# Kernel optimization log

Hardware: AMD Instinct MI355X
Metric: run time of the kernel (lower is better)

Reference implementation:

```python
import jax, jax.numpy as jnp
import numpy as np

B, T_H, N, F_P = 16, 24, 256, 6
H, PRED_LEN, F_W = 64, 12, 4


def _build_static(coords):
    # haversine distance matrix -> gaussian kernel -> threshold (epsilon=0.5)
    lon, lat = coords[:, 0], coords[:, 1]
    dlon = lon[None, :] - lon[:, None]
    dlat = lat[None, :] - lat[:, None]
    a = (np.sin(np.radians(dlat / 2)) ** 2
         + np.cos(np.radians(lat[:, None])) * np.cos(np.radians(lat[None, :]))
         * np.sin(np.radians(dlon / 2)) ** 2)
    dist = 2.0 * 6371.0 * np.arcsin(np.sqrt(np.clip(a, 0.0, None)))
    std = dist.flatten().std()
    adj = np.exp(-np.square(dist / std))
    adj[adj < 0.5] = 0.0
    return adj.astype(np.float32)


def setup_inputs() -> dict:
    key = jax.random.key(0)
    ks = jax.random.split(key, 16)
    rng = np.random.default_rng(0)
    coords_np = np.stack([116.0 + rng.uniform(-1.0, 1.0, N),
                          40.0 + rng.uniform(-1.0, 1.0, N)], axis=1).astype(np.float32)
    s = 0.05
    scale_w = jnp.asarray([1.0, 360.0, 10.0, 1.0], jnp.float32)  # [_, dir(deg), speed, _]
    return {
        "history_pollution": jax.random.normal(ks[0], (B, T_H, N, F_P), jnp.float32),
        "history_weather": jax.random.uniform(ks[1], (B, T_H, F_W), jnp.float32) * scale_w,
        "static_adj": jnp.asarray(_build_static(coords_np)),
        "coords": jnp.asarray(coords_np),
        "w_gc1": jax.random.normal(ks[2], (H, F_P), jnp.float32) * s,
        "b_gc1": jax.random.normal(ks[3], (H,), jnp.float32) * s,
        "w_gc2": jax.random.normal(ks[4], (H, H), jnp.float32) * s,
        "b_gc2": jax.random.normal(ks[5], (H,), jnp.float32) * s,
        "w_ih": jax.random.normal(ks[6], (3 * H, H), jnp.float32) * s,
        "w_hh": jax.random.normal(ks[7], (3 * H, H), jnp.float32) * s,
        "b_ih": jax.random.normal(ks[8], (3 * H,), jnp.float32) * s,
        "b_hh": jax.random.normal(ks[9], (3 * H,), jnp.float32) * s,
        "w_m1": jax.random.normal(ks[10], (32, H), jnp.float32) * s,
        "b_m1": jax.random.normal(ks[11], (32,), jnp.float32) * s,
        "w_m2": jax.random.normal(ks[12], (F_P, 32), jnp.float32) * s,
        "b_m2": jax.random.normal(ks[13], (F_P,), jnp.float32) * s,
    }


def _forward(history_pollution, history_weather, static_adj, coords,
             w_gc1, b_gc1, w_gc2, b_gc2, w_ih, w_hh, b_ih, b_hh,
             w_m1, b_m1, w_m2, b_m2):
    Bs, Th, Ns, Fp = history_pollution.shape
    dt = history_pollution.dtype
    eye = jnp.eye(Ns, dtype=dt)
    # station pair angles: vecs[i,j] = coords[j] - coords[i]
    vecs = coords[None, :, :] - coords[:, None, :]
    ang = jnp.arctan2(vecs[..., 1], vecs[..., 0])  # [N,N]

    def gconv(x, adj, w, b):
        wt = adj + eye[None]                         # [B,N,N]
        d = 1.0 / (jnp.sqrt(wt.sum(-1)) + 1e-6)      # [B,N]
        norm = d[:, :, None] * wt * d[:, None, :]    # D^-1/2 W D^-1/2
        return jnp.einsum('bij,bjf->bif', norm, x) @ w.T + b

    def gcb(x, w_out, w_in):
        h1 = jax.nn.relu(gconv(x, w_out, w_gc1, b_gc1))
        return jax.nn.relu(gconv(h1, w_in, w_gc2, b_gc2))

    def gru(h, x):                                   # h,x: [B*N,H]
        gi = x @ w_ih.T + b_ih
        gh = h @ w_hh.T + b_hh
        i_r, i_z, i_n = jnp.split(gi, 3, axis=-1)
        h_r, h_z, h_n = jnp.split(gh, 3, axis=-1)
        r = jax.nn.sigmoid(i_r + h_r)
        z = jax.nn.sigmoid(i_z + h_z)
        n = jnp.tanh(i_n + r * h_n)
        return (1.0 - z) * n + z * h

    def mlp(x):
        return jax.nn.relu(x @ w_m1.T + b_m1) @ w_m2.T + b_m2

    def enc_step(carry, xs):
        h, _ = carry
        x_t, spd, wd = xs                            # [B,N,F],[B],[B]
        rad = jnp.deg2rad(wd)
        w_dyn = jnp.maximum(spd[:, None, None] * jnp.cos(ang[None] - rad[:, None, None]), 0.0)
        w_out = static_adj[None] * w_dyn             # [B,N,N]
        sf = gcb(x_t, w_out, jnp.swapaxes(w_out, 1, 2))
        h = gru(h, sf.reshape(Bs * Ns, -1))
        return (h, w_out), None

    h0 = jnp.zeros((Bs * Ns, w_hh.shape[1]), dt)
    xs = (jnp.moveaxis(history_pollution, 1, 0),      # [T,B,N,F]
          history_weather[:, :, 2].T,                 # wind speed [T,B]
          history_weather[:, :, 1].T)                 # wind dir   [T,B]
    (h, last_w_out), _ = jax.lax.scan(enc_step, (h0, jnp.zeros((Bs, Ns, Ns), dt)), xs)
    last_w_in = jnp.swapaxes(last_w_out, 1, 2)

    dec0 = mlp(h.reshape(Bs, Ns, -1))

    def dec_step(carry, _):
        h_c, x = carry
        sf = gcb(x, last_w_out, last_w_in)
        h_c = gru(h_c, sf.reshape(Bs * Ns, -1))
        pred = mlp(h_c.reshape(Bs, Ns, -1))
        return (h_c, pred), pred

    _, preds = jax.lax.scan(dec_step, (h, dec0), None, length=PRED_LEN)
    return jnp.moveaxis(preds, 0, 1)                  # [B, pred_len, N, F_P]


def reference(history_pollution, history_weather, static_adj, coords,
              w_gc1, b_gc1, w_gc2, b_gc2, w_ih, w_hh, b_ih, b_hh,
              w_m1, b_m1, w_m2, b_m2):
    return _forward(history_pollution, history_weather, static_adj, coords,
                    w_gc1, b_gc1, w_gc2, b_gc2, w_ih, w_hh, b_ih, b_hh,
                    w_m1, b_m1, w_m2, b_m2)
```

## Files before the change

kernel.cpp:

```cpp
#include <hip/hip_runtime.h>
#include <math.h>

#define Bsz 16
#define Tt 24
#define Nn 256
#define Fp 6
#define Hh 64
#define PredL 12
#define Fw 4
#define M1 32
#define TCHUNK 8
#define DEG2RAD 0.017453292519943295f
#define IDX2(t, b) ((t) * Bsz + (b))

__global__ __launch_bounds__(256) void k_prep(
    const float* __restrict__ coords, const float* __restrict__ adj,
    const float* __restrict__ wgc2, const float* __restrict__ wih,
    const float* __restrict__ whh,  const float* __restrict__ wm1,
    const float* __restrict__ wm2,
    float2* __restrict__ pk,
    float* __restrict__ wgc2T, float* __restrict__ wm1T, float* __restrict__ wm2T,
    float4* __restrict__ wihP, float4* __restrict__ whhP) {
  int tid = threadIdx.x;
  if (blockIdx.x < Nn) {
    int i = blockIdx.x;
    int j = tid;
    float dx = coords[2 * j]     - coords[2 * i];
    float dy = coords[2 * j + 1] - coords[2 * i + 1];
    float ang = atan2f(dy, dx);
    float a = adj[i * Nn + j];
    pk[i * Nn + j] = make_float2(a * cosf(ang), a * sinf(ang));
    return;
  }
  for (int idx = tid; idx < Hh * Hh; idx += 256) {
    int g = idx / Hh, k = idx % Hh;
    wgc2T[k * Hh + g] = wgc2[g * Hh + k];
  }
  for (int idx = tid; idx < M1 * Hh; idx += 256) {
    int m = idx / Hh, k = idx % Hh;
    wm1T[k * M1 + m] = wm1[m * Hh + k];
  }
  for (int idx = tid; idx < Fp * M1; idx += 256) {
    int f = idx / M1, m = idx % M1;
    wm2T[m * Fp + f] = wm2[f * M1 + m];
  }
  for (int idx = tid; idx < Hh * 64; idx += 256) {
    int k = idx >> 6, lane = idx & 63;
    wihP[idx] = make_float4(wih[(0 * 64 + lane) * Hh + k],
                            wih[(1 * 64 + lane) * Hh + k],
                            wih[(2 * 64 + lane) * Hh + k], 0.f);
    whhP[idx] = make_float4(whh[(0 * 64 + lane) * Hh + k],
                            whh[(1 * 64 + lane) * Hh + k],
                            whh[(2 * 64 + lane) * Hh + k], 0.f);
  }
}

__global__ __launch_bounds__(256) void k_deg(
    const float* __restrict__ hw, const float2* __restrict__ pk,
    float* __restrict__ dbuf, float* __restrict__ ebuf) {
  int q  = blockIdx.x & 3;
  int tb = blockIdx.x >> 2;
  int t = tb / Bsz, b = tb % Bsz;
  float spd = hw[(b * Tt + t) * Fw + 2];
  float rad = hw[(b * Tt + t) * Fw + 1] * DEG2RAD;
  float cr = cosf(rad), sr = sinf(rad);
  int w = threadIdx.x >> 6, lane = threadIdx.x & 63;
  for (int m = 0; m < 16; ++m) {
    int i = q * 64 + w * 16 + m;
    float rs = 0.f, cs = 0.f;
#pragma unroll
    for (int c = 0; c < 4; ++c) {
      int j = lane + 64 * c;
      float2 pv = pk[i * Nn + j];
      float val = spd * (pv.x * cr + pv.y * sr);
      rs += fmaxf(val, 0.f);
      cs += (j == i) ? fmaxf(val, 0.f) : fmaxf(-val, 0.f);
    }
#pragma unroll
    for (int off = 32; off; off >>= 1) {
      rs += __shfl_xor(rs, off);
      cs += __shfl_xor(cs, off);
    }
    if (lane == 0) {
      dbuf[IDX2(t, b) * Nn + i] = 1.f / (sqrtf(rs + 1.f) + 1e-6f);
      ebuf[IDX2(t, b) * Nn + i] = 1.f / (sqrtf(cs + 1.f) + 1e-6f);
    }
  }
}

__global__ __launch_bounds__(256) void k_enc(
    const float2* __restrict__ pk, const float* __restrict__ hp,
    const float* __restrict__ hw,
    const float* __restrict__ dbuf, const float* __restrict__ ebuf,
    const float* __restrict__ wgc1, const float* __restrict__ bgc1,
    const float* __restrict__ wgc2T, const float* __restrict__ bgc2,
    float* __restrict__ sf_all) {
  __shared__ __align__(16) float u_s[Nn * 8];
  __shared__ __align__(16) float h1_s[Nn * 68];
  int tb = blockIdx.x, t = tb / Bsz, b = tb % Bsz;
  int i = threadIdx.x;
  float spd = hw[(b * Tt + t) * Fw + 2];
  float rad = hw[(b * Tt + t) * Fw + 1] * DEG2RAD;
  float cr = cosf(rad), sr = sinf(rad);
  const float* drow = dbuf + IDX2(t, b) * Nn;
  float di = drow[i];
  float ei = ebuf[IDX2(t, b) * Nn + i];
  const float* xsrc = hp + (long)(b * Tt + t) * Nn * Fp;
  for (int idx = i; idx < Nn * Fp; idx += 256) {
    int j = idx / Fp, f = idx - j * Fp;
    u_s[j * 8 + f] = drow[j] * xsrc[idx];
  }
  u_s[i * 8 + 6] = 0.f;
  u_s[i * 8 + 7] = 0.f;
  __syncthreads();

  float a0 = 0.f, a1 = 0.f, a2 = 0.f, a3 = 0.f, a4 = 0.f, a5 = 0.f;
#pragma unroll 4
  for (int j = 0; j < Nn; ++j) {
    float2 pv = pk[j * Nn + i];
    float vji = spd * (pv.x * cr + pv.y * sr);
    float wout = (j == i) ? fmaxf(vji, 0.f) : fmaxf(-vji, 0.f);
    float4 ul = *(const float4*)&u_s[j * 8];
    float4 uh = *(const float4*)&u_s[j * 8 + 4];
    a0 += wout * ul.x; a1 += wout * ul.y; a2 += wout * ul.z;
    a3 += wout * ul.w; a4 += wout * uh.x; a5 += wout * uh.y;
  }
  float y0 = di * (a0 + u_s[i * 8 + 0]);
  float y1 = di * (a1 + u_s[i * 8 + 1]);
  float y2v = di * (a2 + u_s[i * 8 + 2]);
  float y3 = di * (a3 + u_s[i * 8 + 3]);
  float y4 = di * (a4 + u_s[i * 8 + 4]);
  float y5 = di * (a5 + u_s[i * 8 + 5]);

#pragma unroll
  for (int g4 = 0; g4 < 16; ++g4) {
    float4 hv;
#pragma unroll
    for (int q = 0; q < 4; ++q) {
      int g = g4 * 4 + q;
      float v = bgc1[g] + wgc1[g * Fp + 0] * y0 + wgc1[g * Fp + 1] * y1 +
                wgc1[g * Fp + 2] * y2v + wgc1[g * Fp + 3] * y3 +
                wgc1[g * Fp + 4] * y4 + wgc1[g * Fp + 5] * y5;
      v = fmaxf(v, 0.f) * ei;
      ((float*)&hv)[q] = v;
    }
    *(float4*)&h1_s[i * 68 + g4 * 4] = hv;
  }
  __syncthreads();

  float z[64];
#pragma unroll
  for (int k = 0; k < 64; ++k) z[k] = 0.f;
#pragma unroll 2
  for (int j = 0; j < Nn; ++j) {
    float2 pv = pk[j * Nn + i];
    float vji = spd * (pv.x * cr + pv.y * sr);
    float wf = fmaxf(vji, 0.f) + ((j == i) ? 1.f : 0.f);
#pragma unroll
    for (int g4 = 0; g4 < 16; ++g4) {
      float4 h4 = *(const float4*)&h1_s[j * 68 + g4 * 4];
      z[g4 * 4 + 0] += wf * h4.x;
      z[g4 * 4 + 1] += wf * h4.y;
      z[g4 * 4 + 2] += wf * h4.z;
      z[g4 * 4 + 3] += wf * h4.w;
    }
  }
#pragma unroll
  for (int k = 0; k < 64; ++k) z[k] *= ei;
  __syncthreads();

#pragma unroll
  for (int c = 0; c < 4; ++c) {
    float s[16];
#pragma unroll
    for (int q = 0; q < 16; ++q) s[q] = bgc2[c * 16 + q];
#pragma unroll
    for (int k = 0; k < 64; ++k) {
      float zk = z[k];
#pragma unroll
      for (int q = 0; q < 16; ++q) s[q] += wgc2T[k * Hh + c * 16 + q] * zk;
    }
#pragma unroll
    for (int q4 = 0; q4 < 4; ++q4) {
      float4 sv = make_float4(fmaxf(s[q4 * 4 + 0], 0.f), fmaxf(s[q4 * 4 + 1], 0.f),
                              fmaxf(s[q4 * 4 + 2], 0.f), fmaxf(s[q4 * 4 + 3], 0.f));
      *(float4*)&h1_s[i * 68 + c * 16 + q4 * 4] = sv;
    }
  }
  __syncthreads();
  long base = (long)IDX2(t, b) * Nn * Hh;
  for (int idx = i; idx < Nn * 16; idx += 256) {
    int j = idx >> 4, g4 = idx & 15;
    *(float4*)&sf_all[base + j * Hh + g4 * 4] = *(const float4*)&h1_s[j * 68 + g4 * 4];
  }
}

__global__ __launch_bounds__(256) void k_gi(
    const float* __restrict__ sf_all, const float4* __restrict__ wihP,
    const float* __restrict__ bih, float* __restrict__ gi, int t0) {
  __shared__ float sf_c[4][16][64];
  int tid = threadIdx.x, w = tid >> 6, lane = tid & 63;
  int rowc0 = blockIdx.x * 64 + w * 16;
  long rowg0 = (long)t0 * (Bsz * Nn) + rowc0;
#pragma unroll
  for (int rr = 0; rr < 16; ++rr)
    sf_c[w][rr][lane] = sf_all[(rowg0 + rr) * Hh + lane];
  float bi_r = bih[lane], bi_z = bih[64 + lane], bi_n = bih[128 + lane];
  float ar[16], az[16], an[16];
#pragma unroll
  for (int rr = 0; rr < 16; ++rr) { ar[rr] = bi_r; az[rr] = bi_z; an[rr] = bi_n; }
#pragma unroll 2
  for (int kb = 0; kb < 16; ++kb) {
    int k0 = kb * 4;
    float4 wi0 = wihP[(k0 + 0) * 64 + lane];
    float4 wi1 = wihP[(k0 + 1) * 64 + lane];
    float4 wi2 = wihP[(k0 + 2) * 64 + lane];
    float4 wi3 = wihP[(k0 + 3) * 64 + lane];
#pragma unroll
    for (int rr = 0; rr < 16; ++rr) {
      const float4 s4 = *(const float4*)&sf_c[w][rr][k0];
      ar[rr] += s4.x * wi0.x + s4.y * wi1.x + s4.z * wi2.x + s4.w * wi3.x;
      az[rr] += s4.x * wi0.y + s4.y * wi1.y + s4.z * wi2.y + s4.w * wi3.y;
      an[rr] += s4.x * wi0.z + s4.y * wi1.z + s4.z * wi2.z + s4.w * wi3.z;
    }
  }
#pragma unroll
// ... 34 lines not shown
    }
#pragma unroll 4
    for (int kb = 0; kb < 16; ++kb) {
      int k0 = kb * 4;
      float4 wh0 = whhP[(k0 + 0) * 64 + lane];
      float4 wh1 = whhP[(k0 + 1) * 64 + lane];
      float4 wh2 = whhP[(k0 + 2) * 64 + lane];
      float4 wh3 = whhP[(k0 + 3) * 64 + lane];
#pragma unroll
      for (int rr = 0; rr < 4; ++rr) {
        const float4 h4 = *(const float4*)&h_s[w * 4 + rr][k0];
        hr[rr] += h4.x * wh0.x + h4.y * wh1.x + h4.z * wh2.x + h4.w * wh3.x;
        hz[rr] += h4.x * wh0.y + h4.y * wh1.y + h4.z * wh2.y + h4.w * wh3.y;
        hn[rr] += h4.x * wh0.z + h4.y * wh1.z + h4.z * wh2.z + h4.w * wh3.z;
      }
    }
#pragma unroll
    for (int rr = 0; rr < 4; ++rr) {
      float rg = 1.f / (1.f + expf(-(gr[rr] + hr[rr])));
      float zg = 1.f / (1.f + expf(-(gz[rr] + hz[rr])));
      float ng = tanhf(gn[rr] + rg * hn[rr]);
      float hv = (1.f - zg) * ng + zg * h_reg[rr];
      h_reg[rr] = hv;
      h_s[w * 4 + rr][lane] = hv;
    }
  }
#pragma unroll
  for (int rr = 0; rr < 4; ++rr)
    hstate[((long)b * Nn + i0 + w * 4 + rr) * Hh + lane] = h_reg[rr];
}

__global__ __launch_bounds__(256) void k_norm_dec(
    const float* __restrict__ hw, const float2* __restrict__ pk,
    const float* __restrict__ dbuf, const float* __restrict__ ebuf,
    float* __restrict__ A1d, float* __restrict__ A2d) {
  int b = blockIdx.x >> 8;
  int i = blockIdx.x & 255;
  int j = threadIdx.x;
  float spd = hw[(b * Tt + (Tt - 1)) * Fw + 2];
  float rad = hw[(b * Tt + (Tt - 1)) * Fw + 1] * DEG2RAD;
  float cr = cosf(rad), sr = sinf(rad);
  const float* drow = dbuf + IDX2(Tt - 1, b) * Nn;
  const float* erow = ebuf + IDX2(Tt - 1, b) * Nn;
  float2 pv = pk[i * Nn + j];
  float val = spd * (pv.x * cr + pv.y * sr);
  float dlt = (j == i) ? 1.f : 0.f;
  float wout = fmaxf(val, 0.f);
  float win  = (j == i) ? wout : fmaxf(-val, 0.f);
  A1d[((long)b * Nn + i) * Nn + j] = drow[i] * (wout + dlt) * drow[j];
  A2d[((long)b * Nn + i) * Nn + j] = erow[i] * (win + dlt) * erow[j];
}

__global__ __launch_bounds__(256) void k_dec0(
    const float* __restrict__ hstate,
    const float* __restrict__ wm1T, const float* __restrict__ bm1,
    const float* __restrict__ wm2T, const float* __restrict__ bm2,
    float* __restrict__ xnext) {
  const int RPB = 16;
  __shared__ float h_lds[RPB][Hh];
  __shared__ float u_lds[RPB][M1];
  int r0 = blockIdx.x * RPB;
  int tid = threadIdx.x;
#pragma unroll
  for (int c = 0; c < (RPB * Hh) / 256; ++c) {
    int idx = tid + c * 256;
    h_lds[idx >> 6][idx & 63] = hstate[(long)r0 * Hh + idx];
  }
  __syncthreads();
#pragma unroll
  for (int rep = 0; rep < 2; ++rep) {
    int idx = tid + rep * 256;
    int row = idx >> 5, m = idx & 31;
    float um = bm1[m];
    for (int k = 0; k < Hh; ++k) um += wm1T[k * M1 + m] * h_lds[row][k];
    u_lds[row][m] = fmaxf(um, 0.f);
  }
  __syncthreads();
  if (tid < RPB * Fp) {
    int row = tid / Fp, f = tid % Fp;
    float pf = bm2[f];
#pragma unroll
    for (int m = 0; m < M1; ++m) pf += wm2T[m * Fp + f] * u_lds[row][m];
    xnext[(r0 + row) * Fp + f] = pf;
  }
}

__global__ __launch_bounds__(256) void k_dstep_A(
    const float* __restrict__ xb, const float* __restrict__ A1d,
    const float* __restrict__ wgc1, const float* __restrict__ bgc1,
    float* __restrict__ h1d) {
  __shared__ float x_lds[Nn * Fp];
  int b = blockIdx.x >> 4;
  int i0 = (blockIdx.x & 15) * 16;
  int tid = threadIdx.x, w = tid >> 6, lane = tid & 63;
  const float* xsrc = xb + (long)b * Nn * Fp;
#pragma unroll
  for (int c = 0; c < 6; ++c) x_lds[tid + 256 * c] = xsrc[tid + 256 * c];
  __syncthreads();
#pragma unroll
  for (int rr = 0; rr < 4; ++rr) {
    int i = i0 + w * 4 + rr;
    const float* arow = A1d + ((long)b * Nn + i) * Nn;
    float acc[Fp] = {0.f, 0.f, 0.f, 0.f, 0.f, 0.f};
#pragma unroll
    for (int c = 0; c < 4; ++c) {
      int j = lane + 64 * c;
      float wt = arow[j];
#pragma unroll
      for (int f = 0; f < Fp; ++f) acc[f] += wt * x_lds[j * Fp + f];
    }
#pragma unroll
    for (int f = 0; f < Fp; ++f) {
#pragma unroll
      for (int off = 32; off; off >>= 1) acc[f] += __shfl_xor(acc[f], off);
    }
    float hv = bgc1[lane];
#pragma unroll
    for (int f = 0; f < Fp; ++f) hv += wgc1[lane * Fp + f] * acc[f];
    h1d[((long)b * Nn + i) * Hh + lane] = fmaxf(hv, 0.f);
  }
}

__global__ __launch_bounds__(256) void k_dstep_B(
    const float* __restrict__ A2d, const float* __restrict__ h1d,
    const float* __restrict__ wgc2T, const float* __restrict__ bgc2,
    const float4* __restrict__ wihP, const float4* __restrict__ whhP,
    const float* __restrict__ bih, const float* __restrict__ bhh,
    float* __restrict__ hstate,
    const float* __restrict__ wm1T, const float* __restrict__ bm1,
    const float* __restrict__ wm2T, const float* __restrict__ bm2,
    float* __restrict__ outp, float* __restrict__ xnext, int p) {
  __shared__ __align__(16) float wvT[Nn * 20];
  __shared__ float red[4][16][Hh];
  __shared__ float y2[16][Hh];
  __shared__ float sf_s[16][Hh];
  __shared__ float h_s[16][Hh];
  __shared__ float hn_lds[16][Hh];
  __shared__ float u_lds[16][M1];
  int b = blockIdx.x >> 4;
  int i0 = (blockIdx.x & 15) * 16;
  int tid = threadIdx.x, w = tid >> 6, lane = tid & 63;

#pragma unroll
  for (int r = 0; r < 16; ++r)
    wvT[tid * 20 + r] = A2d[((long)b * Nn + i0 + r) * Nn + tid];
  float hp_reg[4];
#pragma unroll
  for (int rr = 0; rr < 4; ++rr) {
    hp_reg[rr] = hstate[((long)b * Nn + i0 + w * 4 + rr) * Hh + lane];
    h_s[w * 4 + rr][lane] = hp_reg[rr];
  }
  __syncthreads();

  float acc[16];
#pragma unroll
  for (int r = 0; r < 16; ++r) acc[r] = 0.f;
  const float* h1b = h1d + (long)b * Nn * Hh;
#pragma unroll 4
  for (int jj = 0; jj < 64; ++jj) {
    int j = w * 64 + jj;
    float hv = h1b[j * Hh + lane];
    const float4* wp = (const float4*)(wvT + j * 20);
    float4 w0 = wp[0], w1 = wp[1], w2 = wp[2], w3 = wp[3];
    acc[0] += w0.x * hv; acc[1] += w0.y * hv; acc[2] += w0.z * hv; acc[3] += w0.w * hv;
    acc[4] += w1.x * hv; acc[5] += w1.y * hv; acc[6] += w1.z * hv; acc[7] += w1.w * hv;
    acc[8] += w2.x * hv; acc[9] += w2.y * hv; acc[10] += w2.z * hv; acc[11] += w2.w * hv;
    acc[12] += w3.x * hv; acc[13] += w3.y * hv; acc[14] += w3.z * hv; acc[15] += w3.w * hv;
  }
#pragma unroll
  for (int r = 0; r < 16; ++r) red[w][r][lane] = acc[r];
  __syncthreads();
#pragma unroll
  for (int rr = 0; rr < 4; ++rr) {
    int r = w * 4 + rr;
    y2[r][lane] = red[0][r][lane] + red[1][r][lane] + red[2][r][lane] + red[3][r][lane];
  }
  {
    float a0 = bgc2[lane], a1 = a0, a2 = a0, a3 = a0;
    for (int k = 0; k < Hh; ++k) {
      float wk = wgc2T[k * Hh + lane];
      a0 += wk * y2[w * 4 + 0][k];
      a1 += wk * y2[w * 4 + 1][k];
      a2 += wk * y2[w * 4 + 2][k];
      a3 += wk * y2[w * 4 + 3][k];
    }
    sf_s[w * 4 + 0][lane] = fmaxf(a0, 0.f);
    sf_s[w * 4 + 1][lane] = fmaxf(a1, 0.f);
    sf_s[w * 4 + 2][lane] = fmaxf(a2, 0.f);
    sf_s[w * 4 + 3][lane] = fmaxf(a3, 0.f);
  }

  float hn_reg[4];
  {
    float bi_r = bih[lane], bi_z = bih[64 + lane], bi_n = bih[128 + lane];
    float bh_r = bhh[lane], bh_z = bhh[64 + lane], bh_n = bhh[128 + lane];
    float gir[4], giz[4], gin[4], ghr[4], ghz[4], ghn[4];
#pragma unroll
    for (int rr = 0; rr < 4; ++rr) {
      gir[rr] = bi_r; giz[rr] = bi_z; gin[rr] = bi_n;
      ghr[rr] = bh_r; ghz[rr] = bh_z; ghn[rr] = bh_n;
    }
#pragma unroll 4
    for (int kb = 0; kb < 16; ++kb) {
      int k0 = kb * 4;
      float4 wi[4], wh[4];
#pragma unroll
      for (int q = 0; q < 4; ++q) {
        wi[q] = wihP[(k0 + q) * 64 + lane];
        wh[q] = whhP[(k0 + q) * 64 + lane];
      }
#pragma unroll
      for (int rr = 0; rr < 4; ++rr) {
        const float4 s4 = *(const float4*)&sf_s[w * 4 + rr][k0];
        const float4 h4 = *(const float4*)&h_s[w * 4 + rr][k0];
        gir[rr] += s4.x * wi[0].x + s4.y * wi[1].x + s4.z * wi[2].x + s4.w * wi[3].x;
        giz[rr] += s4.x * wi[0].y + s4.y * wi[1].y + s4.z * wi[2].y + s4.w * wi[3].y;
        gin[rr] += s4.x * wi[0].z + s4.y * wi[1].z + s4.z * wi[2].z + s4.w * wi[3].z;
        ghr[rr] += h4.x * wh[0].x + h4.y * wh[1].x + h4.z * wh[2].x + h4.w * wh[3].x;
        ghz[rr] += h4.x * wh[0].y + h4.y * wh[1].y + h4.z * wh[2].y + h4.w * wh[3].y;
        ghn[rr] += h4.x * wh[0].z + h4.y * wh[1].z + h4.z * wh[2].z + h4.w * wh[3].z;
      }
    }
#pragma unroll
    for (int rr = 0; rr < 4; ++rr) {
      float rg = 1.f / (1.f + expf(-(gir[rr] + ghr[rr])));
      float zg = 1.f / (1.f + expf(-(giz[rr] + ghz[rr])));
      float ng = tanhf(gin[rr] + rg * ghn[rr]);
      hn_reg[rr] = (1.f - zg) * ng + zg * hp_reg[rr];
      hstate[((long)b * Nn + i0 + w * 4 + rr) * Hh + lane] = hn_reg[rr];
      hn_lds[w * 4 + rr][lane] = hn_reg[rr];
    }
  }
  __syncthreads();
#pragma unroll
  for (int rep = 0; rep < 2; ++rep) {
    int idx = tid + rep * 256;
    int row = idx >> 5, m = idx & 31;
    float um = bm1[m];
    for (int k = 0; k < Hh; ++k) um += wm1T[k * M1 + m] * hn_lds[row][k];
    u_lds[row][m] = fmaxf(um, 0.f);
  }
  __syncthreads();
  if (tid < 16 * Fp) {
    int row = tid / Fp, f = tid % Fp;
    float pf = bm2[f];
#pragma unroll
    for (int m = 0; m < M1; ++m) pf += wm2T[m * Fp + f] * u_lds[row][m];
    int i = i0 + row;
    outp[(((long)b * PredL + p) * Nn + i) * Fp + f] = pf;
    xnext[((long)b * Nn + i) * Fp + f] = pf;
  }
}

extern "C" void kernel_launch(void* const* d_in, const int* in_sizes, int n_in,
                              void* d_out, int out_size, void* d_ws, size_t ws_size,
                              hipStream_t stream) {
  const float* hp     = (const float*)d_in[0];
  const float* hw     = (const float*)d_in[1];
  const float* adj    = (const float*)d_in[2];
  const float* coords = (const float*)d_in[3];
  const float* wgc1   = (const float*)d_in[4];
  const float* bgc1   = (const float*)d_in[5];
  const float* wgc2   = (const float*)d_in[6];
  const float* bgc2   = (const float*)d_in[7];
  const float* wih    = (const float*)d_in[8];
  const float* whh    = (const float*)d_in[9];
  const float* bih    = (const float*)d_in[10];
  const float* bhh    = (const float*)d_in[11];
  const float* wm1    = (const float*)d_in[12];
  const float* bm1    = (const float*)d_in[13];
  const float* wm2    = (const float*)d_in[14];
  const float* bm2    = (const float*)d_in[15];
  float* out = (float*)d_out;

  float* w = (float*)d_ws;
  float2* pk    = (float2*)w; w += Nn * Nn * 2;
  float* dbuf   = w; w += Tt * Bsz * Nn;
  float* ebuf   = w; w += Tt * Bsz * Nn;
  float* hstate = w; w += Bsz * Nn * Hh;
  float* sf_all = w; w += (long)Tt * Bsz * Nn * Hh;
  float* gi_ch  = w; w += (long)TCHUNK * Bsz * Nn * 3 * 64;
  float* h1d    = w; w += Bsz * Nn * Hh;
  float* xb0    = w; w += Bsz * Nn * Fp;
  float* xb1    = w; w += Bsz * Nn * Fp;
  float* A1d    = w; w += Bsz * Nn * Nn;
  float* A2d    = w; w += Bsz * Nn * Nn;
  float* wgc2T  = w; w += Hh * Hh;
  float* wm1T   = w; w += Hh * M1;
  float* wm2T   = w; w += M1 * Fp;
  float4* wihP  = (float4*)w; w += Hh * 64 * 4;
  float4* whhP  = (float4*)w; w += Hh * 64 * 4;

  k_prep<<<Nn + 1, 256, 0, stream>>>(coords, adj, wgc2, wih, whh, wm1, wm2,
                                     pk, wgc2T, wm1T, wm2T, wihP, whhP);
  k_deg<<<Tt * Bsz * 4, 256, 0, stream>>>(hw, pk, dbuf, ebuf);

  k_enc<<<Tt * Bsz, 256, 0, stream>>>(pk, hp, hw, dbuf, ebuf,
                                      wgc1, bgc1, wgc2T, bgc2, sf_all);

  for (int s = 0; s < Tt / TCHUNK; ++s) {
    int t0 = s * TCHUNK;
    k_gi<<<(TCHUNK * Bsz * Nn) / 64, 256, 0, stream>>>(sf_all, wihP, bih,
                                                       gi_ch, t0);
    k_gru_scan4<<<Bsz * 16, 256, 0, stream>>>(gi_ch, whhP, bhh, hstate,
                                              t0, TCHUNK);
  }

  k_norm_dec<<<Bsz * Nn, 256, 0, stream>>>(hw, pk, dbuf, ebuf, A1d, A2d);
  k_dec0<<<Bsz * Nn / 16, 256, 0, stream>>>(hstate, wm1T, bm1, wm2T, bm2, xb0);

  for (int p = 0; p < PredL; ++p) {
    float* xin  = (p & 1) ? xb1 : xb0;
    float* xout = (p & 1) ? xb0 : xb1;
    k_dstep_A<<<Bsz * 16, 256, 0, stream>>>(xin, A1d, wgc1, bgc1, h1d);
    k_dstep_B<<<Bsz * 16, 256, 0, stream>>>(
        A2d, h1d, wgc2T, bgc2, wihP, whhP, bih, bhh, hstate,
        wm1T, bm1, wm2T, bm2, out, xout, p);
  }
}
```

Measured before the change: 738.5 us.

## Fuse degree computation into encoder and make decoder a persistent grid-barrier kernel

Folds the per-timestep degree normalisation into the encoder kernel, which now runs 128 threads each handling two nodes and writes the GCN output straight to global memory. It keeps only the last-step degrees for the decoder. The 12-step decoder loop and the initial MLP are merged into one persistent kernel that synchronises across blocks with an atomic-counter grid barrier. The encoder chunk size is raised from 8 to 12. The goal is to cut many kernel launches and a separate degree pass, at the cost of spin-wait barriers that rely on all 256 blocks being resident at once, plus lower encoder occupancy.

Result: slower. 1.190 ms (+61.1%).

```diff
diff --git a/kernel.cpp b/kernel.cpp
--- a/kernel.cpp
+++ b/kernel.cpp
@@ -9,7 +9,7 @@
 #define PredL 12
 #define Fw 4
 #define M1 32
-#define TCHUNK 8
+#define TCHUNK 12
 #define DEG2RAD 0.017453292519943295f
 #define IDX2(t, b) ((t) * Bsz + (b))
 
@@ -20,7 +20,8 @@
     const float* __restrict__ wm2,
     float2* __restrict__ pk,
     float* __restrict__ wgc2T, float* __restrict__ wm1T, float* __restrict__ wm2T,
-    float4* __restrict__ wihP, float4* __restrict__ whhP) {
+    float4* __restrict__ wihP, float4* __restrict__ whhP,
+    unsigned* __restrict__ ctr) {
   int tid = threadIdx.x;
   if (blockIdx.x < Nn) {
     int i = blockIdx.x;
@@ -32,6 +33,7 @@
     pk[i * Nn + j] = make_float2(a * cosf(ang), a * sinf(ang));
     return;
   }
+  if (tid == 0) *ctr = 0u;
   for (int idx = tid; idx < Hh * Hh; idx += 256) {
     int g = idx / Hh, k = idx % Hh;
     wgc2T[k * Hh + g] = wgc2[g * Hh + k];
@@ -55,143 +57,168 @@
   }
 }
 
-__global__ __launch_bounds__(256) void k_deg(
-    const float* __restrict__ hw, const float2* __restrict__ pk,
-    float* __restrict__ dbuf, float* __restrict__ ebuf) {
-  int q  = blockIdx.x & 3;
-  int tb = blockIdx.x >> 2;
-  int t = tb / Bsz, b = tb % Bsz;
+__global__ __launch_bounds__(128, 1) void k_enc(
+    const float2* __restrict__ pk, const float* __restrict__ hp,
+    const float* __restrict__ hw,
+    const float* __restrict__ wgc1, const float* __restrict__ bgc1,
+    const float* __restrict__ wgc2T, const float* __restrict__ bgc2,
+    float* __restrict__ sf_all,
+    float* __restrict__ d23, float* __restrict__ e23) {
+  __shared__ float d_lds[Nn];
+  __shared__ float e_lds[Nn];
+  __shared__ __align__(16) float u_s[Nn * 8];
+  __shared__ __align__(16) float h1_s[Nn * 68];
+  int tb = blockIdx.x, t = tb / Bsz, b = tb % Bsz;
+  int tid = threadIdx.x;
+  int ia = tid, ib = tid + 128;
   float spd = hw[(b * Tt + t) * Fw + 2];
   float rad = hw[(b * Tt + t) * Fw + 1] * DEG2RAD;
   float cr = cosf(rad), sr = sinf(rad);
-  int w = threadIdx.x >> 6, lane = threadIdx.x & 63;
-  for (int m = 0; m < 16; ++m) {
-    int i = q * 64 + w * 16 + m;
-    float rs = 0.f, cs = 0.f;
-#pragma unroll
-    for (int c = 0; c < 4; ++c) {
-      int j = lane + 64 * c;
-      float2 pv = pk[i * Nn + j];
-      float val = spd * (pv.x * cr + pv.y * sr);
-      rs += fmaxf(val, 0.f);
-      cs += (j == i) ? fmaxf(val, 0.f) : fmaxf(-val, 0.f);
-    }
-#pragma unroll
-    for (int off = 32; off; off >>= 1) {
-      rs += __shfl_xor(rs, off);
-      cs += __shfl_xor(cs, off);
-    }
-    if (lane == 0) {
-      dbuf[IDX2(t, b) * Nn + i] = 1.f / (sqrtf(rs + 1.f) + 1e-6f);
-      ebuf[IDX2(t, b) * Nn + i] = 1.f / (sqrtf(cs + 1.f) + 1e-6f);
-    }
-  }
-}
-
-__global__ __launch_bounds__(256) void k_enc(
-    const float2* __restrict__ pk, const float* __restrict__ hp,
-    const float* __restrict__ hw,
-    const float* __restrict__ dbuf, const float* __restrict__ ebuf,
-    const float* __restrict__ wgc1, const float* __restrict__ bgc1,
-    const float* __restrict__ wgc2T, const float* __restrict__ bgc2,
-    float* __restrict__ sf_all) {
-  __shared__ __align__(16) float u_s[Nn * 8];
-  __shared__ __align__(16) float h1_s[Nn * 68];
-  int tb = blockIdx.x, t = tb / Bsz, b = tb % Bsz;
-  int i = threadIdx.x;
-  float spd = hw[(b * Tt + t) * Fw + 2];
-  float rad = hw[(b * Tt + t) * Fw + 1] * DEG2RAD;
-  float cr = cosf(rad), sr = sinf(rad);
-  const float* drow = dbuf + IDX2(t, b) * Nn;
-  float di = drow[i];
-  float ei = ebuf[IDX2(t, b) * Nn + i];
-  const float* xsrc = hp + (long)(b * Tt + t) * Nn * Fp;
-  for (int idx = i; idx < Nn * Fp; idx += 256) {
-    int j = idx / Fp, f = idx - j * Fp;
-    u_s[j * 8 + f] = drow[j] * xsrc[idx];
-  }
-  u_s[i * 8 + 6] = 0.f;
-  u_s[i * 8 + 7] = 0.f;
+
+  {
+    float rs_a = 0.f, cs_a = 0.f, rs_b = 0.f, cs_b = 0.f;
+#pragma unroll 4
+    for (int j = 0; j < Nn; ++j) {
+      float2 pa = pk[j * Nn + ia];
+      float2 pb = pk[j * Nn + ib];
+      float va = spd * (pa.x * cr + pa.y * sr);
+      float vb = spd * (pb.x * cr + pb.y * sr);
+      float vap = fmaxf(va, 0.f), vbp = fmaxf(vb, 0.f);
+      cs_a += vap;
+      cs_b += vbp;
+      rs_a += (j == ia) ? vap : fmaxf(-va, 0.f);
+      rs_b += (j == ib) ? vbp : fmaxf(-vb, 0.f);
+    }
+    d_lds[ia] = 1.f / (sqrtf(rs_a + 1.f) + 1e-6f);
+    d_lds[ib] = 1.f / (sqrtf(rs_b + 1.f) + 1e-6f);
+    e_lds[ia] = 1.f / (sqrtf(cs_a + 1.f) + 1e-6f);
+    e_lds[ib] = 1.f / (sqrtf(cs_b + 1.f) + 1e-6f);
+    if (t == Tt - 1) {
+      d23[b * Nn + ia] = d_lds[ia]; d23[b * Nn + ib] = d_lds[ib];
+      e23[b * Nn + ia] = e_lds[ia]; e23[b * Nn + ib] = e_lds[ib];
+    }
+  }
   __syncthreads();
 
-  float a0 = 0.f, a1 = 0.f, a2 = 0.f, a3 = 0.f, a4 = 0.f, a5 = 0.f;
-#pragma unroll 4
-  for (int j = 0; j < Nn; ++j) {
-    float2 pv = pk[j * Nn + i];
-    float vji = spd * (pv.x * cr + pv.y * sr);
-    float wout = (j == i) ? fmaxf(vji, 0.f) : fmaxf(-vji, 0.f);
-    float4 ul = *(const float4*)&u_s[j * 8];
-    float4 uh = *(const float4*)&u_s[j * 8 + 4];
-    a0 += wout * ul.x; a1 += wout * ul.y; a2 += wout * ul.z;
-    a3 += wout * ul.w; a4 += wout * uh.x; a5 += wout * uh.y;
-  }
-  float y0 = di * (a0 + u_s[i * 8 + 0]);
-  float y1 = di * (a1 + u_s[i * 8 + 1]);
-  float y2v = di * (a2 + u_s[i * 8 + 2]);
-  float y3 = di * (a3 + u_s[i * 8 + 3]);
-  float y4 = di * (a4 + u_s[i * 8 + 4]);
-  float y5 = di * (a5 + u_s[i * 8 + 5]);
+  {
+    const float* xsrc = hp + (long)(b * Tt + t) * Nn * Fp;
+    for (int idx = tid; idx < Nn * Fp; idx += 128) {
+      int j = idx / Fp, f = idx - j * Fp;
+      u_s[j * 8 + f] = d_lds[j] * xsrc[idx];
+    }
+    u_s[ia * 8 + 6] = 0.f; u_s[ia * 8 + 7] = 0.f;
+    u_s[ib * 8 + 6] = 0.f; u_s[ib * 8 + 7] = 0.f;
+  }
+  __syncthreads();
+
+  float da = d_lds[ia], db = d_lds[ib];
+  float ea = e_lds[ia], eb = e_lds[ib];
+
+  float ya[Fp], yb[Fp];
+  {
+    float aa[Fp] = {0, 0, 0, 0, 0, 0}, ab[Fp] = {0, 0, 0, 0, 0, 0};
+#pragma unroll 2
+    for (int j = 0; j < Nn; ++j) {
+      float2 pa = pk[j * Nn + ia];
+      float2 pb = pk[j * Nn + ib];
+      float va = spd * (pa.x * cr + pa.y * sr);
+      float vb = spd * (pb.x * cr + pb.y * sr);
+      float wa = (j == ia) ? fmaxf(va, 0.f) : fmaxf(-va, 0.f);
+      float wb = (j == ib) ? fmaxf(vb, 0.f) : fmaxf(-vb, 0.f);
+      float4 ul = *(const float4*)&u_s[j * 8];
+      float4 uh = *(const float4*)&u_s[j * 8 + 4];
+      aa[0] += wa * ul.x; aa[1] += wa * ul.y; aa[2] += wa * ul.z;
+      aa[3] += wa * ul.w; aa[4] += wa * uh.x; aa[5] += wa * uh.y;
+      ab[0] += wb * ul.x; ab[1] += wb * ul.y; ab[2] += wb * ul.z;
+      ab[3] += wb * ul.w; ab[4] += wb * uh.x; ab[5] += wb * uh.y;
+    }
+#pragma unroll
+    for (int f = 0; f < Fp; ++f) {
+      ya[f] = da * (aa[f] + u_s[ia * 8 + f]);
+      yb[f] = db * (ab[f] + u_s[ib * 8 + f]);
+    }
+  }
 
 #pragma unroll
   for (int g4 = 0; g4 < 16; ++g4) {
-    float4 hv;
+    float4 hva, hvb;
 #pragma unroll
     for (int q = 0; q < 4; ++q) {
       int g = g4 * 4 + q;
-      float v = bgc1[g] + wgc1[g * Fp + 0] * y0 + wgc1[g * Fp + 1] * y1 +
-                wgc1[g * Fp + 2] * y2v + wgc1[g * Fp + 3] * y3 +
-                wgc1[g * Fp + 4] * y4 + wgc1[g * Fp + 5] * y5;
-      v = fmaxf(v, 0.f) * ei;
-      ((float*)&hv)[q] = v;
-    }
-    *(float4*)&h1_s[i * 68 + g4 * 4] = hv;
+      float va = bgc1[g], vb = va;
+#pragma unroll
+      for (int f = 0; f < Fp; ++f) {
+        float wg = wgc1[g * Fp + f];
+        va += wg * ya[f];
+        vb += wg * yb[f];
+      }
+      ((float*)&hva)[q] = fmaxf(va, 0.f) * ea;
+      ((float*)&hvb)[q] = fmaxf(vb, 0.f) * eb;
+    }
+    *(float4*)&h1_s[ia * 68 + g4 * 4] = hva;
+    *(float4*)&h1_s[ib * 68 + g4 * 4] = hvb;
   }
   __syncthreads();
 
-  float z[64];
-#pragma unroll
-  for (int k = 0; k < 64; ++k) z[k] = 0.f;
+  float4 za[16], zb[16];
+#pragma unroll
+  for (int q = 0; q < 16; ++q) {
+    za[q] = make_float4(0.f, 0.f, 0.f, 0.f);
+    zb[q] = make_float4(0.f, 0.f, 0.f, 0.f);
+  }
 #pragma unroll 2
   for (int j = 0; j < Nn; ++j) {
-    float2 pv = pk[j * Nn + i];
-    float vji = spd * (pv.x * cr + pv.y * sr);
-    float wf = fmaxf(vji, 0.f) + ((j == i) ? 1.f : 0.f);
+    float2 pa = pk[j * Nn + ia];
+    float2 pb = pk[j * Nn + ib];
+    float va = spd * (pa.x * cr + pa.y * sr);
+    float vb = spd * (pb.x * cr + pb.y * sr);
+    float wfa = fmaxf(va, 0.f) + ((j == ia) ? 1.f : 0.f);
+    float wfb = fmaxf(vb, 0.f) + ((j == ib) ? 1.f : 0.f);
 #pragma unroll
     for (int g4 = 0; g4 < 16; ++g4) {
       float4 h4 = *(const float4*)&h1_s[j * 68 + g4 * 4];
-      z[g4 * 4 + 0] += wf * h4.x;
-      z[g4 * 4 + 1] += wf * h4.y;
-      z[g4 * 4 + 2] += wf * h4.z;
-      z[g4 * 4 + 3] += wf * h4.w;
-    }
-  }
-#pragma unroll
-  for (int k = 0; k < 64; ++k) z[k] *= ei;
-  __syncthreads();
-
+      za[g4].x += wfa * h4.x; za[g4].y += wfa * h4.y;
+      za[g4].z += wfa * h4.z; za[g4].w += wfa * h4.w;
+      zb[g4].x += wfb * h4.x; zb[g4].y += wfb * h4.y;
+      zb[g4].z += wfb * h4.z; zb[g4].w += wfb * h4.w;
+    }
+  }
+#pragma unroll
+  for (int q = 0; q < 16; ++q) {
+    za[q].x *= ea; za[q].y *= ea; za[q].z *= ea; za[q].w *= ea;
+    zb[q].x *= eb; zb[q].y *= eb; zb[q].z *= eb; zb[q].w *= eb;
+  }
+
+  long base = (long)IDX2(t, b) * Nn * Hh;
 #pragma unroll
   for (int c = 0; c < 4; ++c) {
-    float s[16];
-#pragma unroll
-    for (int q = 0; q < 16; ++q) s[q] = bgc2[c * 16 + q];
-#pragma unroll
-    for (int k = 0; k < 64; ++k) {
-      float zk = z[k];
-#pragma unroll
-      for (int q = 0; q < 16; ++q) s[q] += wgc2T[k * Hh + c * 16 + q] * zk;
+    float sa[16], sb[16];
+#pragma unroll
+    for (int q = 0; q < 16; ++q) { sa[q] = bgc2[c * 16 + q]; sb[q] = sa[q]; }
+#pragma unroll
+    for (int k4 = 0; k4 < 16; ++k4) {
+#pragma unroll
+      for (int e = 0; e < 4; ++e) {
+        int k = k4 * 4 + e;
+        float zka = ((const float*)&za[k4])[e];
+        float zkb = ((const float*)&zb[k4])[e];
+#pragma unroll
+        for (int q = 0; q < 16; ++q) {
+          float wk = wgc2T[k * Hh + c * 16 + q];
+          sa[q] += wk * zka;
+          sb[q] += wk * zkb;
+        }
+      }
     }
 #pragma unroll
     for (int q4 = 0; q4 < 4; ++q4) {
-      float4 sv = make_float4(fmaxf(s[q4 * 4 + 0], 0.f), fmaxf(s[q4 * 4 + 1], 0.f),
-                              fmaxf(s[q4 * 4 + 2], 0.f), fmaxf(s[q4 * 4 + 3], 0.f));
-      *(float4*)&h1_s[i * 68 + c * 16 + q4 * 4] = sv;
-    }
-  }
-  __syncthreads();
-  long base = (long)IDX2(t, b) * Nn * Hh;
-  for (int idx = i; idx < Nn * 16; idx += 256) {
-    int j = idx >> 4, g4 = idx & 15;
-    *(float4*)&sf_all[base + j * Hh + g4 * 4] = *(const float4*)&h1_s[j * 68 + g4 * 4];
+      float4 va = make_float4(fmaxf(sa[q4 * 4 + 0], 0.f), fmaxf(sa[q4 * 4 + 1], 0.f),
+                              fmaxf(sa[q4 * 4 + 2], 0.f), fmaxf(sa[q4 * 4 + 3], 0.f));
+      float4 vb = make_float4(fmaxf(sb[q4 * 4 + 0], 0.f), fmaxf(sb[q4 * 4 + 1], 0.f),
+                              fmaxf(sb[q4 * 4 + 2], 0.f), fmaxf(sb[q4 * 4 + 3], 0.f));
+      *(float4*)&sf_all[base + (long)ia * Hh + c * 16 + q4 * 4] = va;
+      *(float4*)&sf_all[base + (long)ib * Hh + c * 16 + q4 * 4] = vb;
+    }
   }
 }
 
@@ -292,7 +319,7 @@
 
 __global__ __launch_bounds__(256) void k_norm_dec(
     const float* __restrict__ hw, const float2* __restrict__ pk,
-    const float* __restrict__ dbuf, const float* __restrict__ ebuf,
+    const float* __restrict__ d23, const float* __restrict__ e23,
     float* __restrict__ A1d, float* __restrict__ A2d) {
   int b = blockIdx.x >> 8;
   int i = blockIdx.x & 255;
@@ -300,8 +327,8 @@
   float spd = hw[(b * Tt + (Tt - 1)) * Fw + 2];
   float rad = hw[(b * Tt + (Tt - 1)) * Fw + 1] * DEG2RAD;
   float cr = cosf(rad), sr = sinf(rad);
-  const float* drow = dbuf + IDX2(Tt - 1, b) * Nn;
-  const float* erow = ebuf + IDX2(Tt - 1, b) * Nn;
+  const float* drow = d23 + b * Nn;
+  const float* erow = e23 + b * Nn;
   float2 pv = pk[i * Nn + j];
   float val = spd * (pv.x * cr + pv.y * sr);
   float dlt = (j == i) ? 1.f : 0.f;
@@ -311,95 +338,42 @@
   A2d[((long)b * Nn + i) * Nn + j] = erow[i] * (win + dlt) * erow[j];
 }
 
-__global__ __launch_bounds__(256) void k_dec0(
+__device__ __forceinline__ void gridbar(unsigned* ctr, unsigned* tgt) {
+  __syncthreads();
+  *tgt += 256u;
+  if (threadIdx.x == 0) {
+    __threadfence();
+    __hip_atomic_fetch_add(ctr, 1u, __ATOMIC_RELEASE, __HIP_MEMORY_SCOPE_AGENT);
+    while (__hip_atomic_load(ctr, __ATOMIC_ACQUIRE, __HIP_MEMORY_SCOPE_AGENT) < *tgt)
+      __builtin_amdgcn_s_sleep(2);
+  }
+  __syncthreads();
+}
+
+__global__ __launch_bounds__(256) void k_decoder(
+    const float* __restrict__ A1d, const float* __restrict__ A2d,
+    float* __restrict__ h1d, float* __restrict__ xb0, float* __restrict__ xb1,
     const float* __restrict__ hstate,
+    const float4* __restrict__ wihP, const float4* __restrict__ whhP,
+    const float* __restrict__ wgc2T, const float* __restrict__ wgc1,
+    const float* __restrict__ bgc1, const float* __restrict__ bgc2,
+    const float* __restrict__ bih, const float* __restrict__ bhh,
     const float* __restrict__ wm1T, const float* __restrict__ bm1,
     const float* __restrict__ wm2T, const float* __restrict__ bm2,
-    float* __restrict__ xnext) {
-  const int RPB = 16;
-  __shared__ float h_lds[RPB][Hh];
-  __shared__ float u_lds[RPB][M1];
-  int r0 = blockIdx.x * RPB;
-  int tid = threadIdx.x;
-#pragma unroll
-  for (int c = 0; c < (RPB * Hh) / 256; ++c) {
-    int idx = tid + c * 256;
-    h_lds[idx >> 6][idx & 63] = hstate[(long)r0 * Hh + idx];
-  }
-  __syncthreads();
-#pragma unroll
-  for (int rep = 0; rep < 2; ++rep) {
-    int idx = tid + rep * 256;
-    int row = idx >> 5, m = idx & 31;
-    float um = bm1[m];
-    for (int k = 0; k < Hh; ++k) um += wm1T[k * M1 + m] * h_lds[row][k];
-    u_lds[row][m] = fmaxf(um, 0.f);
-  }
-  __syncthreads();
-  if (tid < RPB * Fp) {
-    int row = tid / Fp, f = tid % Fp;
-    float pf = bm2[f];
-#pragma unroll
-    for (int m = 0; m < M1; ++m) pf += wm2T[m * Fp + f] * u_lds[row][m];
-    xnext[(r0 + row) * Fp + f] = pf;
-  }
-}
-
-__global__ __launch_bounds__(256) void k_dstep_A(
-    const float* __restrict__ xb, const float* __restrict__ A1d,
-    const float* __restrict__ wgc1, const float* __restrict__ bgc1,
-    float* __restrict__ h1d) {
+    float* __restrict__ outp, unsigned* __restrict__ ctr) {
+  __shared__ __align__(16) float wvT[Nn * 20];
   __shared__ float x_lds[Nn * Fp];
-  int b = blockIdx.x >> 4;
-  int i0 = (blockIdx.x & 15) * 16;
-  int tid = threadIdx.x, w = tid >> 6, lane = tid & 63;
-  const float* xsrc = xb + (long)b * Nn * Fp;
-#pragma unroll
-  for (int c = 0; c < 6; ++c) x_lds[tid + 256 * c] = xsrc[tid + 256 * c];
-  __syncthreads();
-#pragma unroll
-  for (int rr = 0; rr < 4; ++rr) {
-    int i = i0 + w * 4 + rr;
-    const float* arow = A1d + ((long)b * Nn + i) * Nn;
-    float acc[Fp] = {0.f, 0.f, 0.f, 0.f, 0.f, 0.f};
-#pragma unroll
-    for (int c = 0; c < 4; ++c) {
-      int j = lane + 64 * c;
-      float wt = arow[j];
-#pragma unroll
-      for (int f = 0; f < Fp; ++f) acc[f] += wt * x_lds[j * Fp + f];
-    }
-#pragma unroll
-    for (int f = 0; f < Fp; ++f) {
-#pragma unroll
-      for (int off = 32; off; off >>= 1) acc[f] += __shfl_xor(acc[f], off);
-    }
-    float hv = bgc1[lane];
-#pragma unroll
-    for (int f = 0; f < Fp; ++f) hv += wgc1[lane * Fp + f] * acc[f];
-    h1d[((long)b * Nn + i) * Hh + lane] = fmaxf(hv, 0.f);
-  }
-}
-
-__global__ __launch_bounds__(256) void k_dstep_B(
-    const float* __restrict__ A2d, const float* __restrict__ h1d,
-    const float* __restrict__ wgc2T, const float* __restrict__ bgc2,
-    const float4* __restrict__ wihP, const float4* __restrict__ whhP,
-    const float* __restrict__ bih, const float* __restrict__ bhh,
-    float* __restrict__ hstate,
-    const float* __restrict__ wm1T, const float* __restrict__ bm1,
-    const float* __restrict__ wm2T, const float* __restrict__ bm2,
-    float* __restrict__ outp, float* __restrict__ xnext, int p) {
-  __shared__ __align__(16) float wvT[Nn * 20];
   __shared__ float red[4][16][Hh];
   __shared__ float y2[16][Hh];
   __shared__ float sf_s[16][Hh];
   __shared__ float h_s[16][Hh];
   __shared__ float hn_lds[16][Hh];
   __shared__ float u_lds[16][M1];
+
   int b = blockIdx.x >> 4;
   int i0 = (blockIdx.x & 15) * 16;
   int tid = threadIdx.x, w = tid >> 6, lane = tid & 63;
+  unsigned tgt = 0u;
 
 #pragma unroll
   for (int r = 0; r < 16; ++r)
@@ -409,89 +383,12 @@
   for (int rr = 0; rr < 4; ++rr) {
     hp_reg[rr] = hstate[((long)b * Nn + i0 + w * 4 + rr) * Hh + lane];
     h_s[w * 4 + rr][lane] = hp_reg[rr];
-  }
+    hn_lds[w * 4 + rr][lane] = hp_reg[rr];
+  }
+  float bi_r = bih[lane], bi_z = bih[64 + lane], bi_n = bih[128 + lane];
+  float bh_r = bhh[lane], bh_z = bhh[64 + lane], bh_n = bhh[128 + lane];
   __syncthreads();
 
-  float acc[16];
-#pragma unroll
-  for (int r = 0; r < 16; ++r) acc[r] = 0.f;
-  const float* h1b = h1d + (long)b * Nn * Hh;
-#pragma unroll 4
-  for (int jj = 0; jj < 64; ++jj) {
-    int j = w * 64 + jj;
-    float hv = h1b[j * Hh + lane];
-    const float4* wp = (const float4*)(wvT + j * 20);
-    float4 w0 = wp[0], w1 = wp[1], w2 = wp[2], w3 = wp[3];
-    acc[0] += w0.x * hv; acc[1] += w0.y * hv; acc[2] += w0.z * hv; acc[3] += w0.w * hv;
-    acc[4] += w1.x * hv; acc[5] += w1.y * hv; acc[6] += w1.z * hv; acc[7] += w1.w * hv;
-    acc[8] += w2.x * hv; acc[9] += w2.y * hv; acc[10] += w2.z * hv; acc[11] += w2.w * hv;
-    acc[12] += w3.x * hv; acc[13] += w3.y * hv; acc[14] += w3.z * hv; acc[15] += w3.w * hv;
-  }
-#pragma unroll
-  for (int r = 0; r < 16; ++r) red[w][r][lane] = acc[r];
-  __syncthreads();
-#pragma unroll
-  for (int rr = 0; rr < 4; ++rr) {
-    int r = w * 4 + rr;
-    y2[r][lane] = red[0][r][lane] + red[1][r][lane] + red[2][r][lane] + red[3][r][lane];
-  }
-  {
-    float a0 = bgc2[lane], a1 = a0, a2 = a0, a3 = a0;
-    for (int k = 0; k < Hh; ++k) {
-      float wk = wgc2T[k * Hh + lane];
-      a0 += wk * y2[w * 4 + 0][k];
-      a1 += wk * y2[w * 4 + 1][k];
-      a2 += wk * y2[w * 4 + 2][k];
-      a3 += wk * y2[w * 4 + 3][k];
-    }
-    sf_s[w * 4 + 0][lane] = fmaxf(a0, 0.f);
-    sf_s[w * 4 + 1][lane] = fmaxf(a1, 0.f);
-    sf_s[w * 4 + 2][lane] = fmaxf(a2, 0.f);
-    sf_s[w * 4 + 3][lane] = fmaxf(a3, 0.f);
-  }
-
-  float hn_reg[4];
-  {
-    float bi_r = bih[lane], bi_z = bih[64 + lane], bi_n = bih[128 + lane];
-    float bh_r = bhh[lane], bh_z = bhh[64 + lane], bh_n = bhh[128 + lane];
-    float gir[4], giz[4], gin[4], ghr[4], ghz[4], ghn[4];
-#pragma unroll
-    for (int rr = 0; rr < 4; ++rr) {
-      gir[rr] = bi_r; giz[rr] = bi_z; gin[rr] = bi_n;
-      ghr[rr] = bh_r; ghz[rr] = bh_z; ghn[rr] = bh_n;
-    }
-#pragma unroll 4
-    for (int kb = 0; kb < 16; ++kb) {
-      int k0 = kb * 4;
-      float4 wi[4], wh[4];
-#pragma unroll
-      for (int q = 0; q < 4; ++q) {
-        wi[q] = wihP[(k0 + q) * 64 + lane];
-        wh[q] = whhP[(k0 + q) * 64 + lane];
-      }
-#pragma unroll
-      for (int rr = 0; rr < 4; ++rr) {
-        const float4 s4 = *(const float4*)&sf_s[w * 4 + rr][k0];
-        const float4 h4 = *(const float4*)&h_s[w * 4 + rr][k0];
-        gir[rr] += s4.x * wi[0].x + s4.y * wi[1].x + s4.z * wi[2].x + s4.w * wi[3].x;
-        giz[rr] += s4.x * wi[0].y + s4.y * wi[1].y + s4.z * wi[2].y + s4.w * wi[3].y;
-        gin[rr] += s4.x * wi[0].z + s4.y * wi[1].z + s4.z * wi[2].z + s4.w * wi[3].z;
-        ghr[rr] += h4.x * wh[0].x + h4.y * wh[1].x + h4.z * wh[2].x + h4.w * wh[3].x;
-        ghz[rr] += h4.x * wh[0].y + h4.y * wh[1].y + h4.z * wh[2].y + h4.w * wh[3].y;
-        ghn[rr] += h4.x * wh[0].z + h4.y * wh[1].z + h4.z * wh[2].z + h4.w * wh[3].z;
-      }
-    }
-#pragma unroll
-    for (int rr = 0; rr < 4; ++rr) {
-      float rg = 1.f / (1.f + expf(-(gir[rr] + ghr[rr])));
-      float zg = 1.f / (1.f + expf(-(giz[rr] + ghz[rr])));
-      float ng = tanhf(gin[rr] + rg * ghn[rr]);
-      hn_reg[rr] = (1.f - zg) * ng + zg * hp_reg[rr];
-      hstate[((long)b * Nn + i0 + w * 4 + rr) * Hh + lane] = hn_reg[rr];
-      hn_lds[w * 4 + rr][lane] = hn_reg[rr];
-    }
-  }
-  __syncthreads();
 #pragma unroll
   for (int rep = 0; rep < 2; ++rep) {
     int idx = tid + rep * 256;
@@ -506,9 +403,141 @@
     float pf = bm2[f];
 #pragma unroll
     for (int m = 0; m < M1; ++m) pf += wm2T[m * Fp + f] * u_lds[row][m];
-    int i = i0 + row;
-    outp[(((long)b * PredL + p) * Nn + i) * Fp + f] = pf;
-    xnext[((long)b * Nn + i) * Fp + f] = pf;
+    xb0[((long)b * Nn + i0 + row) * Fp + f] = pf;
+  }
+  gridbar(ctr, &tgt);
+
+  for (int p = 0; p < PredL; ++p) {
+    const float* xin = (p & 1) ? xb1 : xb0;
+    float* xout      = (p & 1) ? xb0 : xb1;
+
+    for (int idx = tid; idx < Nn * Fp; idx += 256)
+      x_lds[idx] = xin[(long)b * Nn * Fp + idx];
+    __syncthreads();
+#pragma unroll
+    for (int rr = 0; rr < 4; ++rr) {
+      int i = i0 + w * 4 + rr;
+      const float* arow = A1d + ((long)b * Nn + i) * Nn;
+      float acc[Fp] = {0.f, 0.f, 0.f, 0.f, 0.f, 0.f};
+#pragma unroll
+      for (int c = 0; c < 4; ++c) {
+        int j = lane + 64 * c;
+        float wt = arow[j];
+#pragma unroll
+        for (int f = 0; f < Fp; ++f) acc[f] += wt * x_lds[j * Fp + f];
+      }
+#pragma unroll
+      for (int f = 0; f < Fp; ++f) {
+#pragma unroll
+        for (int off = 32; off; off >>= 1) acc[f] += __shfl_xor(acc[f], off);
+      }
+      float hv = bgc1[lane];
+#pragma unroll
+      for (int f = 0; f < Fp; ++f) hv += wgc1[lane * Fp + f] * acc[f];
+      h1d[((long)b * Nn + i) * Hh + lane] = fmaxf(hv, 0.f);
+    }
+    gridbar(ctr, &tgt);
+
+    float acc[16];
+#pragma unroll
+    for (int r = 0; r < 16; ++r) acc[r] = 0.f;
+    const float* h1b = h1d + (long)b * Nn * Hh;
+#pragma unroll 4
+    for (int jj = 0; jj < 64; ++jj) {
+      int j = w * 64 + jj;
+      float hv = h1b[j * Hh + lane];
+      const float4* wp = (const float4*)(wvT + j * 20);
+      float4 w0 = wp[0], w1 = wp[1], w2 = wp[2], w3 = wp[3];
+      acc[0] += w0.x * hv; acc[1] += w0.y * hv; acc[2] += w0.z * hv; acc[3] += w0.w * hv;
+      acc[4] += w1.x * hv; acc[5] += w1.y * hv; acc[6] += w1.z * hv; acc[7] += w1.w * hv;
+      acc[8] += w2.x * hv; acc[9] += w2.y * hv; acc[10] += w2.z * hv; acc[11] += w2.w * hv;
+      acc[12] += w3.x * hv; acc[13] += w3.y * hv; acc[14] += w3.z * hv; acc[15] += w3.w * hv;
+    }
+#pragma unroll
+    for (int r = 0; r < 16; ++r) red[w][r][lane] = acc[r];
+    __syncthreads();
+#pragma unroll
+    for (int rr = 0; rr < 4; ++rr) {
+      int r = w * 4 + rr;
+      y2[r][lane] = red[0][r][lane] + red[1][r][lane] + red[2][r][lane] + red[3][r][lane];
+    }
+    {
+      float a0 = bgc2[lane], a1 = a0, a2 = a0, a3 = a0;
+      for (int k = 0; k < Hh; ++k) {
+        float wk = wgc2T[k * Hh + lane];
+        a0 += wk * y2[w * 4 + 0][k];
+        a1 += wk * y2[w * 4 + 1][k];
+        a2 += wk * y2[w * 4 + 2][k];
+        a3 += wk * y2[w * 4 + 3][k];
+      }
+      sf_s[w * 4 + 0][lane] = fmaxf(a0, 0.f);
+      sf_s[w * 4 + 1][lane] = fmaxf(a1, 0.f);
+      sf_s[w * 4 + 2][lane] = fmaxf(a2, 0.f);
+      sf_s[w * 4 + 3][lane] = fmaxf(a3, 0.f);
+    }
+    {
+      float gir[4], giz[4], gin[4], ghr[4], ghz[4], ghn[4];
+#pragma unroll
+      for (int rr = 0; rr < 4; ++rr) {
+        gir[rr] = bi_r; giz[rr] = bi_z; gin[rr] = bi_n;
+        ghr[rr] = bh_r; ghz[rr] = bh_z; ghn[rr] = bh_n;
+      }
+#pragma unroll 4
+      for (int kb = 0; kb < 16; ++kb) {
+        int k0 = kb * 4;
+        float4 wi[4], wh[4];
+#pragma unroll
+        for (int q = 0; q < 4; ++q) {
+          wi[q] = wihP[(k0 + q) * 64 + lane];
+          wh[q] = whhP[(k0 + q) * 64 + lane];
+        }
+#pragma unroll
+        for (int rr = 0; rr < 4; ++rr) {
+          const float4 s4 = *(const float4*)&sf_s[w * 4 + rr][k0];
+          const float4 h4 = *(const float4*)&h_s[w * 4 + rr][k0];
+          gir[rr] += s4.x * wi[0].x + s4.y * wi[1].x + s4.z * wi[2].x + s4.w * wi[3].x;
+          giz[rr] += s4.x * wi[0].y + s4.y * wi[1].y + s4.z * wi[2].y + s4.w * wi[3].y;
+          gin[rr] += s4.x * wi[0].z + s4.y * wi[1].z + s4.z * wi[2].z + s4.w * wi[3].z;
+          ghr[rr] += h4.x * wh[0].x + h4.y * wh[1].x + h4.z * wh[2].x + h4.w * wh[3].x;
+          ghz[rr] += h4.x * wh[0].y + h4.y * wh[1].y + h4.z * wh[2].y + h4.w * wh[3].y;
+          ghn[rr] += h4.x * wh[0].z + h4.y * wh[1].z + h4.z * wh[2].z + h4.w * wh[3].z;
+        }
+      }
+#pragma unroll
+      for (int rr = 0; rr < 4; ++rr) {
+        float rg = 1.f / (1.f + expf(-(gir[rr] + ghr[rr])));
+        float zg = 1.f / (1.f + expf(-(giz[rr] + ghz[rr])));
+        float ng = tanhf(gin[rr] + rg * ghn[rr]);
+        float hn = (1.f - zg) * ng + zg * hp_reg[rr];
+        hp_reg[rr] = hn;
+      }
+    }
+    __syncthreads();
+#pragma unroll
+    for (int rr = 0; rr < 4; ++rr) {
+      h_s[w * 4 + rr][lane] = hp_reg[rr];
+      hn_lds[w * 4 + rr][lane] = hp_reg[rr];
+    }
+    __syncthreads();
+#pragma unroll
+    for (int rep = 0; rep < 2; ++rep) {
+      int idx = tid + rep * 256;
+      int row = idx >> 5, m = idx & 31;
+      float um = bm1[m];
+      for (int k = 0; k < Hh; ++k) um += wm1T[k * M1 + m] * hn_lds[row][k];
+      u_lds[row][m] = fmaxf(um, 0.f);
+    }
+    __syncthreads();
+    if (tid < 16 * Fp) {
+      int row = tid / Fp, f = tid % Fp;
+      float pf = bm2[f];
+#pragma unroll
+      for (int m = 0; m < M1; ++m) pf += wm2T[m * Fp + f] * u_lds[row][m];
+      int i = i0 + row;
+      outp[(((long)b * PredL + p) * Nn + i) * Fp + f] = pf;
+      xout[((long)b * Nn + i) * Fp + f] = pf;
+    }
+    gridbar(ctr, &tgt);
   }
 }
 
@@ -535,8 +564,8 @@
 
   float* w = (float*)d_ws;
   float2* pk    = (float2*)w; w += Nn * Nn * 2;
-  float* dbuf   = w; w += Tt * Bsz * Nn;
-  float* ebuf   = w; w += Tt * Bsz * Nn;
+  float* d23    = w; w += Bsz * Nn;
+  float* e23    = w; w += Bsz * Nn;
   float* hstate = w; w += Bsz * Nn * Hh;
   float* sf_all = w; w += (long)Tt * Bsz * Nn * Hh;
   float* gi_ch  = w; w += (long)TCHUNK * Bsz * Nn * 3 * 64;
@@ -550,14 +579,12 @@
   float* wm2T   = w; w += M1 * Fp;
   float4* wihP  = (float4*)w; w += Hh * 64 * 4;
   float4* whhP  = (float4*)w; w += Hh * 64 * 4;
+  unsigned* ctr = (unsigned*)w; w += 4;
 
   k_prep<<<Nn + 1, 256, 0, stream>>>(coords, adj, wgc2, wih, whh, wm1, wm2,
-                                     pk, wgc2T, wm1T, wm2T, wihP, whhP);
-  k_deg<<<Tt * Bsz * 4, 256, 0, stream>>>(hw, pk, dbuf, ebuf);
-
-  k_enc<<<Tt * Bsz, 256, 0, stream>>>(pk, hp, hw, dbuf, ebuf,
-                                      wgc1, bgc1, wgc2T, bgc2, sf_all);
-
+                                     pk, wgc2T, wm1T, wm2T, wihP, whhP, ctr);
+  k_enc<<<Tt * Bsz, 128, 0, stream>>>(pk, hp, hw, wgc1, bgc1, wgc2T, bgc2,
+                                      sf_all, d23, e23);
   for (int s = 0; s < Tt / TCHUNK; ++s) {
     int t0 = s * TCHUNK;
     k_gi<<<(TCHUNK * Bsz * Nn) / 64, 256, 0, stream>>>(sf_all, wihP, bih,
@@ -565,16 +592,9 @@
     k_gru_scan4<<<Bsz * 16, 256, 0, stream>>>(gi_ch, whhP, bhh, hstate,
                                               t0, TCHUNK);
   }
-
-  k_norm_dec<<<Bsz * Nn, 256, 0, stream>>>(hw, pk, dbuf, ebuf, A1d, A2d);
-  k_dec0<<<Bsz * Nn / 16, 256, 0, stream>>>(hstate, wm1T, bm1, wm2T, bm2, xb0);
-
-  for (int p = 0; p < PredL; ++p) {
-    float* xin  = (p & 1) ? xb1 : xb0;
-    float* xout = (p & 1) ? xb0 : xb1;
-    k_dstep_A<<<Bsz * 16, 256, 0, stream>>>(xin, A1d, wgc1, bgc1, h1d);
-    k_dstep_B<<<Bsz * 16, 256, 0, stream>>>(
-        A2d, h1d, wgc2T, bgc2, wihP, whhP, bih, bhh, hstate,
-        wm1T, bm1, wm2T, bm2, out, xout, p);
-  }
-}
+  k_norm_dec<<<Bsz * Nn, 256, 0, stream>>>(hw, pk, d23, e23, A1d, A2d);
+
+  k_decoder<<<Bsz * 16, 256, 0, stream>>>(
+      A1d, A2d, h1d, xb0, xb1, hstate, wihP, whhP, wgc2T, wgc1, bgc1, bgc2,
+      bih, bhh, wm1T, bm1, wm2T, bm2, out, ctr);
+}
```
